# Performance work log

Measured on AMD Instinct MI355X. Metric: run time of the kernel, lower is better.

## Reference

```python
import jax, jax.numpy as jnp
import numpy as np

# ---- static configuration (mirrors scalar_python args) ----
N_SHOTS = 8
NZ = NX = 300
FD_PAD = 2                 # accuracy 4 -> fd_pad = accuracy // 2
NZP = NZ + 2 * FD_PAD      # 304
NXP = NX + 2 * FD_PAD      # 304
NT = 50
N_SRC = 1
N_REC = 300
DT = 0.001
DX = 4.0
INV_DX = 1.0 / DX
INV_DX2 = 1.0 / (DX * DX)
FLAT = NZP * NXP


def _shift(x, axis, s):
    """result[i] = x[i + s] along `axis`, zero-filled outside (matches padded-grid stencil)."""
    n = x.shape[axis]
    pad = [(0, 0)] * x.ndim
    if s > 0:
        xs = jax.lax.slice_in_dim(x, s, n, axis=axis)
        pad[axis] = (0, s)
    else:
        xs = jax.lax.slice_in_dim(x, 0, n + s, axis=axis)
        pad[axis] = (-s, 0)
    return jnp.pad(xs, pad)


def diff1(x, axis):
    """4th-order accurate central first derivative * (1/dx)."""
    return ((_shift(x, axis, 1) - _shift(x, axis, -1)) * (2.0 / 3.0)
            + (_shift(x, axis, -2) - _shift(x, axis, 2)) * (1.0 / 12.0)) * INV_DX


def diff2(x, axis):
    """4th-order accurate central second derivative * (1/dx^2)."""
    return ((-2.5) * x
            + (4.0 / 3.0) * (_shift(x, axis, 1) + _shift(x, axis, -1))
            - (1.0 / 12.0) * (_shift(x, axis, 2) + _shift(x, axis, -2))) * INV_DX2


def _forward_step(v2dt2, wfc, wfp, psi, zeta, a, b, dbdx):
    """One FDTD time step with PML (faithful to deepwave _forward_step, ndim=2)."""
    new_psi, new_zeta = [], []
    w_sum = jnp.zeros_like(wfc)
    for dim in range(2):          # dim 0 = z (axis 1), dim 1 = x (axis 2)
        axis = dim + 1
        dudx = diff1(wfc, axis)
        tmp = ((1.0 + b[dim]) * diff2(wfc, axis)
               + dbdx[dim] * dudx
               + diff1(a[dim] * psi[dim], axis))
        w_sum = w_sum + (1.0 + b[dim]) * tmp + a[dim] * zeta[dim]
        new_psi.append(b[dim] * dudx + a[dim] * psi[dim])
        new_zeta.append(b[dim] * tmp + a[dim] * zeta[dim])
    wfc_new = v2dt2 * w_sum + 2.0 * wfc - wfp
    return wfc_new, new_psi, new_zeta


def setup_inputs() -> dict:
    key = jax.random.key(0)
    ks = jax.random.split(key, 10)
    v = 1500.0 + 1000.0 * jax.random.uniform(ks[0], (NZP, NXP), jnp.float32)
    source_amplitudes = jax.random.normal(ks[1], (NT, N_SHOTS, N_SRC), jnp.float32)
    # PML profiles: (a, b, dbdx) per spatial dim, broadcastable 1D profiles.
    a_z = -0.1 * jax.random.uniform(ks[2], (NZP, 1), jnp.float32)
    b_z = 0.1 * jax.random.uniform(ks[3], (NZP, 1), jnp.float32)
    dbdx_z = 0.01 * jax.random.normal(ks[4], (NZP, 1), jnp.float32)
    a_x = -0.1 * jax.random.uniform(ks[5], (1, NXP), jnp.float32)
    b_x = 0.1 * jax.random.uniform(ks[6], (1, NXP), jnp.float32)
    dbdx_x = 0.01 * jax.random.normal(ks[7], (1, NXP), jnp.float32)
    sources_i = jax.random.randint(ks[8], (N_SHOTS, N_SRC), 0, FLAT, jnp.int32)
    receivers_i = jax.random.randint(ks[9], (N_SHOTS, N_REC), 0, FLAT, jnp.int32)
    return {"v": v, "source_amplitudes": source_amplitudes,
            "a_z": a_z, "b_z": b_z, "dbdx_z": dbdx_z,
            "a_x": a_x, "b_x": b_x, "dbdx_x": dbdx_x,
            "sources_i": sources_i, "receivers_i": receivers_i}


def reference(v, source_amplitudes, a_z, b_z, dbdx_z, a_x, b_x, dbdx_x,
              sources_i, receivers_i):
    v2dt2 = (v * v) * (DT * DT)                 # (NZP, NXP), broadcasts over shots
    a = (a_z, a_x)
    b = (b_z, b_x)
    dbdx = (dbdx_z, dbdx_x)
    shot_idx = jnp.arange(N_SHOTS)[:, None]
    zeros = jnp.zeros((N_SHOTS, NZP, NXP), v.dtype)

    def body(carry, amp_t):
        wfc, wfp, pz, px, zz, zx = carry
        # record receivers from the current wavefield (before the step)
        rec = jnp.take_along_axis(wfc.reshape(N_SHOTS, -1), receivers_i, axis=1)
        wfc_new, (pzn, pxn), (zzn, zxn) = _forward_step(
            v2dt2, wfc, wfp, (pz, px), (zz, zx), a, b, dbdx)
        # inject sources into the new wavefield (scatter-add of flat indices)
        flat = wfc_new.reshape(N_SHOTS, -1).at[shot_idx, sources_i].add(amp_t)
        wfc_new = flat.reshape(N_SHOTS, NZP, NXP)
        return (wfc_new, wfc, pzn, pxn, zzn, zxn), rec

    init = (zeros, zeros, zeros, zeros, zeros, zeros)
    _, receiver_amplitudes = jax.lax.scan(body, init, source_amplitudes)
    return receiver_amplitudes   # (NT, N_SHOTS, N_REC)
```

## Files before the change

kernel.cpp:

```cpp
#include <hip/hip_runtime.h>

#define N_SHOTS 8
#define NZP 304
#define NXP 304
#define NT 50
#define N_REC 300
#define FLAT (NZP * NXP)
#define DT 0.001f
#define INV_DX 0.25f
#define INV_DX2 0.0625f

#define C23 (2.0f / 3.0f)
#define C112 (1.0f / 12.0f)
#define C43 (4.0f / 3.0f)

__global__ __launch_bounds__(320) void fdtd_step(
    const float* __restrict__ v,
    const float* __restrict__ amp,
    const float* __restrict__ az, const float* __restrict__ bz, const float* __restrict__ dbz,
    const float* __restrict__ ax, const float* __restrict__ bx, const float* __restrict__ dbx,
    const int* __restrict__ src_i,
    const int* __restrict__ rec_i,
    const float* __restrict__ wfc,
    float* __restrict__ wfp,
    const float* __restrict__ pzin, float* __restrict__ pzout,
    const float* __restrict__ pxin, float* __restrict__ pxout,
    float* __restrict__ zzeta, float* __restrict__ xzeta,
    float* __restrict__ rec_out,
    int t)
{
    const int bid = blockIdx.x;
    const int shot = bid & 7;
    const int z = bid >> 3;
    const int tid = threadIdx.x;

    if (tid >= NXP) {
        int gidx = bid * 16 + (tid - NXP);
        if (gidx < N_SHOTS * N_REC) {
            int rshot = gidx / N_REC;
            rec_out[t * (N_SHOTS * N_REC) + gidx] =
                wfc[rshot * FLAT + rec_i[gidx]];
        }
        return;
    }

    const int x = tid;
    const int idx = shot * FLAT + z * NXP + x;

    const float c = wfc[idx];

    float xm1 = 0.f, xm2 = 0.f, xp1 = 0.f, xp2 = 0.f;
    float apxm1 = 0.f, apxm2 = 0.f, apxp1 = 0.f, apxp2 = 0.f;
    if (x >= 1)       { xm1 = wfc[idx - 1]; apxm1 = ax[x - 1] * pxin[idx - 1]; }
    if (x >= 2)       { xm2 = wfc[idx - 2]; apxm2 = ax[x - 2] * pxin[idx - 2]; }
    if (x < NXP - 1)  { xp1 = wfc[idx + 1]; apxp1 = ax[x + 1] * pxin[idx + 1]; }
    if (x < NXP - 2)  { xp2 = wfc[idx + 2]; apxp2 = ax[x + 2] * pxin[idx + 2]; }

    float zm1 = 0.f, zm2 = 0.f, zp1 = 0.f, zp2 = 0.f;
    float apzm1 = 0.f, apzm2 = 0.f, apzp1 = 0.f, apzp2 = 0.f;
    if (z >= 1)       { zm1 = wfc[idx - NXP];     apzm1 = az[z - 1] * pzin[idx - NXP]; }
    if (z >= 2)       { zm2 = wfc[idx - 2 * NXP]; apzm2 = az[z - 2] * pzin[idx - 2 * NXP]; }
    if (z < NZP - 1)  { zp1 = wfc[idx + NXP];     apzp1 = az[z + 1] * pzin[idx + NXP]; }
    if (z < NZP - 2)  { zp2 = wfc[idx + 2 * NXP]; apzp2 = az[z + 2] * pzin[idx + 2 * NXP]; }

    const float az_ = az[z], bz_ = bz[z], dbz_ = dbz[z];
    const float d1z = ((zp1 - zm1) * C23 + (zm2 - zp2) * C112) * INV_DX;
    const float d2z = (-2.5f * c + C43 * (zp1 + zm1) - C112 * (zp2 + zm2)) * INV_DX2;
    const float dapz = ((apzp1 - apzm1) * C23 + (apzm2 - apzp2) * C112) * INV_DX;
    const float tmpz = (1.f + bz_) * d2z + dbz_ * d1z + dapz;
    const float zz_c = zzeta[idx];
    const float pz_c = pzin[idx];
    float w_sum = (1.f + bz_) * tmpz + az_ * zz_c;

    const float ax_ = ax[x], bx_ = bx[x], dbx_ = dbx[x];
    const float d1x = ((xp1 - xm1) * C23 + (xm2 - xp2) * C112) * INV_DX;
    const float d2x = (-2.5f * c + C43 * (xp1 + xm1) - C112 * (xp2 + xm2)) * INV_DX2;
    const float dapx = ((apxp1 - apxm1) * C23 + (apxm2 - apxp2) * C112) * INV_DX;
    const float tmpx = (1.f + bx_) * d2x + dbx_ * d1x + dapx;
    const float zx_c = xzeta[idx];
    const float px_c = pxin[idx];
    w_sum += (1.f + bx_) * tmpx + ax_ * zx_c;

    const float vv = v[z * NXP + x];
    float wn = (vv * vv) * (DT * DT) * w_sum + 2.f * c - wfp[idx];

    if (z * NXP + x == src_i[shot])
        wn += amp[t * N_SHOTS + shot];

    wfp[idx]   = wn;
    pzout[idx] = bz_ * d1z + az_ * pz_c;
    pxout[idx] = bx_ * d1x + ax_ * px_c;
    zzeta[idx] = bz_ * tmpz + az_ * zz_c;
    xzeta[idx] = bx_ * tmpx + ax_ * zx_c;
}

extern "C" void kernel_launch(void* const* d_in, const int* in_sizes, int n_in,
                              void* d_out, int out_size, void* d_ws, size_t ws_size,
                              hipStream_t stream) {
    const float* v     = (const float*)d_in[0];
    const float* amp   = (const float*)d_in[1];
    const float* az    = (const float*)d_in[2];
    const float* bz    = (const float*)d_in[3];
    const float* dbz   = (const float*)d_in[4];
    const float* ax    = (const float*)d_in[5];
    const float* bx    = (const float*)d_in[6];
    const float* dbx   = (const float*)d_in[7];
    const int* src_i   = (const int*)d_in[8];
    const int* rec_i   = (const int*)d_in[9];
    float* out = (float*)d_out;

    float* ws = (float*)d_ws;
    const size_t A = (size_t)N_SHOTS * FLAT;

    float* wf[2] = { ws + 0 * A, ws + 1 * A };
    float* pz[2] = { ws + 2 * A, ws + 3 * A };
    float* px[2] = { ws + 4 * A, ws + 5 * A };
    float* zz    = ws + 6 * A;
    float* zx    = ws + 7 * A;

    hipMemsetAsync(d_ws, 0, 8 * A * sizeof(float), stream);

    int cur = 0;
    for (int t = 0; t < NT; ++t) {
        fdtd_step<<<N_SHOTS * NZP, 320, 0, stream>>>(
            v, amp, az, bz, dbz, ax, bx, dbx, src_i, rec_i,
            wf[cur], wf[1 - cur],
            pz[cur], pz[1 - cur],
            px[cur], px[1 - cur],
            zz, zx, out, t);
        cur ^= 1;
    }
}
```

Measured before the change: 453.7 us.

## Vectorize FDTD step to four x-points per thread with float4 loads

Each thread now computes four consecutive x points using float4 loads and stores, and each block covers four z rows instead of one, so the grid shrinks from 2432 to 608 blocks. Horizontal stencil neighbours come from adjacent float4s held in registers, and the receiver gather is remapped per shot across blocks. The workspace is reordered so the zero memset covers only the six buffers read at step zero rather than all eight. The aim is fewer, wider memory transactions and less redundant index arithmetic, at the cost of more registers per thread and fewer blocks in flight.

```diff
diff --git a/kernel.cpp b/kernel.cpp
--- a/kernel.cpp
+++ b/kernel.cpp
@@ -14,84 +14,136 @@
 #define C112 (1.0f / 12.0f)
 #define C43 (4.0f / 3.0f)
 
-__global__ __launch_bounds__(320) void fdtd_step(
+union F4 { float4 v; float f[4]; };
+
+__device__ __forceinline__ F4 ldf4(const float* p) {
+    F4 r; r.v = *reinterpret_cast<const float4*>(p); return r;
+}
+__device__ __forceinline__ F4 zf4() {
+    F4 r; r.v = make_float4(0.f, 0.f, 0.f, 0.f); return r;
+}
+
+__global__ __launch_bounds__(320) void fdtd_step4(
     const float* __restrict__ v,
     const float* __restrict__ amp,
     const float* __restrict__ az, const float* __restrict__ bz, const float* __restrict__ dbz,
     const float* __restrict__ ax, const float* __restrict__ bx, const float* __restrict__ dbx,
     const int* __restrict__ src_i,
     const int* __restrict__ rec_i,
-    const float* __restrict__ wfc,
-    float* __restrict__ wfp,
-    const float* __restrict__ pzin, float* __restrict__ pzout,
-    const float* __restrict__ pxin, float* __restrict__ pxout,
-    float* __restrict__ zzeta, float* __restrict__ xzeta,
+    const float* __restrict__ wc,
+    float* __restrict__ wp,
+    const float* __restrict__ pzi, float* __restrict__ pzo,
+    const float* __restrict__ pxi, float* __restrict__ pxo,
+    float* __restrict__ zz, float* __restrict__ zx,
     float* __restrict__ rec_out,
     int t)
 {
     const int bid = blockIdx.x;
     const int shot = bid & 7;
-    const int z = bid >> 3;
+    const int jg = bid >> 3;
     const int tid = threadIdx.x;
 
-    if (tid >= NXP) {
-        int gidx = bid * 16 + (tid - NXP);
-        if (gidx < N_SHOTS * N_REC) {
-            int rshot = gidx / N_REC;
-            rec_out[t * (N_SHOTS * N_REC) + gidx] =
-                wfc[rshot * FLAT + rec_i[gidx]];
+    if (tid >= 304) {
+        if (jg < 19) {
+            int ridx = jg * 16 + (tid - 304);
+            if (ridx < N_REC) {
+                rec_out[t * (N_SHOTS * N_REC) + shot * N_REC + ridx] =
+                    wc[shot * FLAT + rec_i[shot * N_REC + ridx]];
+            }
         }
         return;
     }
 
-    const int x = tid;
-    const int idx = shot * FLAT + z * NXP + x;
+    const int r = tid / 76;
+    const int i = tid - r * 76;
+    const int z = jg * 4 + r;
+    const int x0 = 4 * i;
+    const int idx = shot * FLAT + z * NXP + x0;
 
-    const float c = wfc[idx];
+    const bool lok = (i > 0), rok = (i < 75);
+    F4 wCx = ldf4(wc + idx);
+    F4 wLx = lok ? ldf4(wc + idx - 4) : zf4();
+    F4 wRx = rok ? ldf4(wc + idx + 4) : zf4();
+    F4 pCx = ldf4(pxi + idx);
+    F4 pLx = lok ? ldf4(pxi + idx - 4) : zf4();
+    F4 pRx = rok ? ldf4(pxi + idx + 4) : zf4();
+    F4 aCx = ldf4(ax + x0);
+    F4 aLx = lok ? ldf4(ax + x0 - 4) : zf4();
+    F4 aRx = rok ? ldf4(ax + x0 + 4) : zf4();
 
-    float xm1 = 0.f, xm2 = 0.f, xp1 = 0.f, xp2 = 0.f;
-    float apxm1 = 0.f, apxm2 = 0.f, apxp1 = 0.f, apxp2 = 0.f;
-    if (x >= 1)       { xm1 = wfc[idx - 1]; apxm1 = ax[x - 1] * pxin[idx - 1]; }
-    if (x >= 2)       { xm2 = wfc[idx - 2]; apxm2 = ax[x - 2] * pxin[idx - 2]; }
-    if (x < NXP - 1)  { xp1 = wfc[idx + 1]; apxp1 = ax[x + 1] * pxin[idx + 1]; }
-    if (x < NXP - 2)  { xp2 = wfc[idx + 2]; apxp2 = ax[x + 2] * pxin[idx + 2]; }
+    float wx[12], apx[12];
+    #pragma unroll
+    for (int k = 0; k < 4; ++k) {
+        wx[k]     = wLx.f[k];  apx[k]     = aLx.f[k] * pLx.f[k];
+        wx[4 + k] = wCx.f[k];  apx[4 + k] = aCx.f[k] * pCx.f[k];
+        wx[8 + k] = wRx.f[k];  apx[8 + k] = aRx.f[k] * pRx.f[k];
+    }
 
-    float zm1 = 0.f, zm2 = 0.f, zp1 = 0.f, zp2 = 0.f;
-    float apzm1 = 0.f, apzm2 = 0.f, apzp1 = 0.f, apzp2 = 0.f;
-    if (z >= 1)       { zm1 = wfc[idx - NXP];     apzm1 = az[z - 1] * pzin[idx - NXP]; }
-    if (z >= 2)       { zm2 = wfc[idx - 2 * NXP]; apzm2 = az[z - 2] * pzin[idx - 2 * NXP]; }
-    if (z < NZP - 1)  { zp1 = wfc[idx + NXP];     apzp1 = az[z + 1] * pzin[idx + NXP]; }
-    if (z < NZP - 2)  { zp2 = wfc[idx + 2 * NXP]; apzp2 = az[z + 2] * pzin[idx + 2 * NXP]; }
+    const bool m1 = (z >= 1), m2 = (z >= 2), p1 = (z < NZP - 1), p2 = (z < NZP - 2);
+    F4 wzm1 = m1 ? ldf4(wc + idx - NXP)     : zf4();
+    F4 wzm2 = m2 ? ldf4(wc + idx - 2 * NXP) : zf4();
+    F4 wzp1 = p1 ? ldf4(wc + idx + NXP)     : zf4();
+    F4 wzp2 = p2 ? ldf4(wc + idx + 2 * NXP) : zf4();
+    const float azm1 = m1 ? az[z - 1] : 0.f;
+    const float azm2 = m2 ? az[z - 2] : 0.f;
+    const float azp1 = p1 ? az[z + 1] : 0.f;
+    const float azp2 = p2 ? az[z + 2] : 0.f;
+    F4 qzm1 = m1 ? ldf4(pzi + idx - NXP)     : zf4();
+    F4 qzm2 = m2 ? ldf4(pzi + idx - 2 * NXP) : zf4();
+    F4 qzp1 = p1 ? ldf4(pzi + idx + NXP)     : zf4();
+    F4 qzp2 = p2 ? ldf4(pzi + idx + 2 * NXP) : zf4();
+    #pragma unroll
+    for (int k = 0; k < 4; ++k) {
+        qzm1.f[k] *= azm1; qzm2.f[k] *= azm2;
+        qzp1.f[k] *= azp1; qzp2.f[k] *= azp2;
+    }
 
-    const float az_ = az[z], bz_ = bz[z], dbz_ = dbz[z];
-    const float d1z = ((zp1 - zm1) * C23 + (zm2 - zp2) * C112) * INV_DX;
-    const float d2z = (-2.5f * c + C43 * (zp1 + zm1) - C112 * (zp2 + zm2)) * INV_DX2;
-    const float dapz = ((apzp1 - apzm1) * C23 + (apzm2 - apzp2) * C112) * INV_DX;
-    const float tmpz = (1.f + bz_) * d2z + dbz_ * d1z + dapz;
-    const float zz_c = zzeta[idx];
-    const float pz_c = pzin[idx];
-    float w_sum = (1.f + bz_) * tmpz + az_ * zz_c;
+    F4 pzC = ldf4(pzi + idx);
+    F4 zzC = ldf4(zz + idx);
+    F4 zxC = ldf4(zx + idx);
+    F4 vC  = ldf4(v + z * NXP + x0);
+    F4 wpC = ldf4(wp + idx);
+    F4 bxC = ldf4(bx + x0);
+    F4 dxC = ldf4(dbx + x0);
+    const float azc = az[z], bzc = bz[z], dbzc = dbz[z];
+    const int srci = src_i[shot];
+    const float amp_t = amp[t * N_SHOTS + shot];
 
-    const float ax_ = ax[x], bx_ = bx[x], dbx_ = dbx[x];
-    const float d1x = ((xp1 - xm1) * C23 + (xm2 - xp2) * C112) * INV_DX;
-    const float d2x = (-2.5f * c + C43 * (xp1 + xm1) - C112 * (xp2 + xm2)) * INV_DX2;
-    const float dapx = ((apxp1 - apxm1) * C23 + (apxm2 - apxp2) * C112) * INV_DX;
-    const float tmpx = (1.f + bx_) * d2x + dbx_ * d1x + dapx;
-    const float zx_c = xzeta[idx];
-    const float px_c = pxin[idx];
-    w_sum += (1.f + bx_) * tmpx + ax_ * zx_c;
+    F4 o_w, o_pz, o_px, o_zz, o_zx;
 
-    const float vv = v[z * NXP + x];
-    float wn = (vv * vv) * (DT * DT) * w_sum + 2.f * c - wfp[idx];
+    #pragma unroll
+    for (int k = 0; k < 4; ++k) {
+        const float c = wx[4 + k];
+        const float d1x  = ((wx[5 + k] - wx[3 + k]) * C23 + (wx[2 + k] - wx[6 + k]) * C112) * INV_DX;
+        const float d2x  = (-2.5f * c + C43 * (wx[5 + k] + wx[3 + k]) - C112 * (wx[6 + k] + wx[2 + k])) * INV_DX2;
+        const float dapx = ((apx[5 + k] - apx[3 + k]) * C23 + (apx[2 + k] - apx[6 + k]) * C112) * INV_DX;
+        const float d1z  = ((wzp1.f[k] - wzm1.f[k]) * C23 + (wzm2.f[k] - wzp2.f[k]) * C112) * INV_DX;
+        const float d2z  = (-2.5f * c + C43 * (wzp1.f[k] + wzm1.f[k]) - C112 * (wzp2.f[k] + wzm2.f[k])) * INV_DX2;
+        const float dapz = ((qzp1.f[k] - qzm1.f[k]) * C23 + (qzm2.f[k] - qzp2.f[k]) * C112) * INV_DX;
 
-    if (z * NXP + x == src_i[shot])
-        wn += amp[t * N_SHOTS + shot];
+        const float tmpz = (1.f + bzc) * d2z + dbzc * d1z + dapz;
+        float w_sum = (1.f + bzc) * tmpz + azc * zzC.f[k];
 
-    wfp[idx]   = wn;
-    pzout[idx] = bz_ * d1z + az_ * pz_c;
-    pxout[idx] = bx_ * d1x + ax_ * px_c;
-    zzeta[idx] = bz_ * tmpz + az_ * zz_c;
-    xzeta[idx] = bx_ * tmpx + ax_ * zx_c;
+        const float bxk = bxC.f[k], axk = aCx.f[k];
+        const float tmpx = (1.f + bxk) * d2x + dxC.f[k] * d1x + dapx;
+        w_sum += (1.f + bxk) * tmpx + axk * zxC.f[k];
+
+        const float vv = vC.f[k];
+        float wn = (vv * vv) * (DT * DT) * w_sum + 2.f * c - wpC.f[k];
+        if (z * NXP + x0 + k == srci) wn += amp_t;
+
+        o_w.f[k]  = wn;
+        o_pz.f[k] = bzc * d1z + azc * pzC.f[k];
+        o_px.f[k] = bxk * d1x + apx[4 + k];
+        o_zz.f[k] = bzc * tmpz + azc * zzC.f[k];
+        o_zx.f[k] = bxk * tmpx + axk * zxC.f[k];
+    }
+
+    *reinterpret_cast<float4*>(wp + idx)  = o_w.v;
+    *reinterpret_cast<float4*>(pzo + idx) = o_pz.v;
+    *reinterpret_cast<float4*>(pxo + idx) = o_px.v;
+    *reinterpret_cast<float4*>(zz + idx)  = o_zz.v;
+    *reinterpret_cast<float4*>(zx + idx)  = o_zx.v;
 }
 
 extern "C" void kernel_launch(void* const* d_in, const int* in_sizes, int n_in,
@@ -112,17 +164,20 @@
     float* ws = (float*)d_ws;
     const size_t A = (size_t)N_SHOTS * FLAT;
 
-    float* wf[2] = { ws + 0 * A, ws + 1 * A };
-    float* pz[2] = { ws + 2 * A, ws + 3 * A };
-    float* px[2] = { ws + 4 * A, ws + 5 * A };
-    float* zz    = ws + 6 * A;
-    float* zx    = ws + 7 * A;
+    float* wf0 = ws + 0 * A; float* wf1 = ws + 1 * A;
+    float* pz0 = ws + 2 * A; float* px0 = ws + 3 * A;
+    float* zz  = ws + 4 * A; float* zx  = ws + 5 * A;
+    float* pz1 = ws + 6 * A; float* px1 = ws + 7 * A;
 
-    hipMemsetAsync(d_ws, 0, 8 * A * sizeof(float), stream);
+    hipMemsetAsync(d_ws, 0, 6 * A * sizeof(float), stream);
+
+    float* wf[2] = { wf0, wf1 };
+    float* pz[2] = { pz0, pz1 };
+    float* px[2] = { px0, px1 };
 
     int cur = 0;
     for (int t = 0; t < NT; ++t) {
-        fdtd_step<<<N_SHOTS * NZP, 320, 0, stream>>>(
+        fdtd_step4<<<8 * 76, 320, 0, stream>>>(
             v, amp, az, bz, dbz, ax, bx, dbx, src_i, rec_i,
             wf[cur], wf[1 - cur],
             pz[cur], pz[1 - cur],
```

After: 434.1 us. -4.3%, faster.
